# Performance work log

Hardware: AMD Instinct MI355X
Metric: run time of the kernel (lower is better)

## Reference

```python
import jax, jax.numpy as jnp
import numpy as np

N_NODES = 100000
N_EDGES = 1600000
NODE_DIM = 128
EDGE_DIM = 48
GLOBAL_DIM = 64
N_GRAPHS = 64
HIDDEN = 256


def setup_inputs() -> dict:
    key = jax.random.key(0)
    ks = jax.random.split(key, 9)
    nodes = jax.random.normal(ks[0], (N_NODES, NODE_DIM), dtype=jnp.float32)
    edges = jax.random.normal(ks[1], (N_EDGES, EDGE_DIM), dtype=jnp.float32)
    edge_index = jax.random.randint(ks[2], (2, N_EDGES), 0, N_NODES, dtype=jnp.int64)
    batch = jnp.sort(jax.random.randint(ks[3], (N_NODES,), 0, N_GRAPHS, dtype=jnp.int64))
    graph_globals = jax.random.normal(ks[4], (N_GRAPHS, GLOBAL_DIM), dtype=jnp.float32)
    in_dim = NODE_DIM + EDGE_DIM + GLOBAL_DIM
    s1 = 1.0 / np.sqrt(in_dim)
    s2 = 1.0 / np.sqrt(HIDDEN)
    W1 = jax.random.uniform(ks[5], (in_dim, HIDDEN), minval=-s1, maxval=s1, dtype=jnp.float32)
    b1 = jax.random.uniform(ks[6], (HIDDEN,), minval=-s1, maxval=s1, dtype=jnp.float32)
    W2 = jax.random.uniform(ks[7], (HIDDEN, NODE_DIM), minval=-s2, maxval=s2, dtype=jnp.float32)
    b2 = jax.random.uniform(ks[8], (NODE_DIM,), minval=-s2, maxval=s2, dtype=jnp.float32)
    return {"nodes": nodes, "edges": edges, "edge_index": edge_index, "batch": batch,
            "graph_globals": graph_globals, "W1": W1, "b1": b1, "W2": W2, "b2": b2}


def reference(nodes, edges, edge_index, batch, graph_globals, W1, b1, W2, b2):
    recv = edge_index[1]
    # scatter-add edge messages to receiving nodes: [N, edge_dim]
    agg = jax.ops.segment_sum(edges, recv, num_segments=N_NODES)
    # gather per-graph globals to nodes: [N, global_dim]
    u = graph_globals[batch]
    x = jnp.concatenate([nodes, agg, u], axis=1)  # [N, node+edge+global]
    h = jax.nn.relu(x @ W1 + b1)
    return h @ W2 + b2  # new node features [N, node_dim]
```

## Files before the change

kernel.cpp:

```cpp
#include <hip/hip_runtime.h>
#include <hip/hip_bf16.h>
#include <stdint.h>

#define N_NODES   100000
#define N_EDGES   1600000
#define NODE_DIM  128
#define EDGE_DIM  48
#define GLOBAL_DIM 64
#define HIDDEN    256
#define KDIM      256
#define OUT_DIM   128

#define N_PAD     100352
#define SCAN_BLKS 98

#define W1P_OFF   0
#define W1P_BYTES (KDIM * HIDDEN * 2)
#define W2P_OFF   (W1P_OFF + W1P_BYTES)
#define W2P_BYTES (HIDDEN * OUT_DIM * 2)
#define CNT_OFF   (W2P_OFF + W2P_BYTES)
#define CNT_BYTES (N_PAD * 4)
#define OFF_OFF   (CNT_OFF + CNT_BYTES)
#define BSUM_OFF  (OFF_OFF + CNT_BYTES)
#define BSUM_BYTES 512
#define BEX_OFF   (BSUM_OFF + BSUM_BYTES)
#define RANK_OFF  (BEX_OFF + BSUM_BYTES)
#define RANK_BYTES (N_EDGES * 4)
#define EIDS_OFF  (RANK_OFF + RANK_BYTES)

typedef short  short4_t  __attribute__((ext_vector_type(4)));
typedef short  short8_t  __attribute__((ext_vector_type(8)));
typedef float  floatx4   __attribute__((ext_vector_type(4)));

__device__ __forceinline__ short f2bf(float f) {
    union { float f; uint32_t u; } x; x.f = f;
    uint32_t r = (x.u + 0x7FFFu + ((x.u >> 16) & 1u)) >> 16;
    return (short)r;
}

__global__ void pack_w1(const float* __restrict__ W1, short* __restrict__ dst) {
    int tid = blockIdx.x * 256 + threadIdx.x;
    int k = tid >> 8, n = tid & 255;
    float v = (k < 240) ? W1[k * 256 + n] : 0.0f;
    int kg = k >> 5, kr = k & 31, quad = kr >> 3, j = kr & 7;
    int nt = n >> 4, nl = n & 15, lane = (quad << 4) | nl;
    dst[(((kg * 16 + nt) * 64) + lane) * 8 + j] = f2bf(v);
}

__global__ void pack_w2(const float* __restrict__ W2, short* __restrict__ dst) {
    int tid = blockIdx.x * 256 + threadIdx.x;
    int k = tid >> 7, n = tid & 127;
    float v = W2[k * 128 + n];
    int kg = k >> 5, kr = k & 31, quad = kr >> 3, j = kr & 7;
    int nt = n >> 4, nl = n & 15, lane = (quad << 4) | nl;
    dst[(((kg * 8 + nt) * 64) + lane) * 8 + j] = f2bf(v);
}

__global__ void count_kernel(const int4* __restrict__ recv4, int* __restrict__ cnt,
                             int4* __restrict__ rank4) {
    int tid = blockIdx.x * 256 + threadIdx.x;
    if (tid >= N_EDGES / 4) return;
    int4 r = recv4[tid];
    int4 k;
    k.x = atomicAdd(&cnt[r.x], 1);
    k.y = atomicAdd(&cnt[r.y], 1);
    k.z = atomicAdd(&cnt[r.z], 1);
    k.w = atomicAdd(&cnt[r.w], 1);
    rank4[tid] = k;
}

__global__ void scan_bsum(const int4* __restrict__ cnt4, int* __restrict__ bsum) {
    int4 v = cnt4[blockIdx.x * 256 + threadIdx.x];
    int s = v.x + v.y + v.z + v.w;
    #pragma unroll
    for (int d = 32; d; d >>= 1) s += __shfl_down(s, d);
    __shared__ int ws[4];
    if ((threadIdx.x & 63) == 0) ws[threadIdx.x >> 6] = s;
    __syncthreads();
    if (threadIdx.x == 0) bsum[blockIdx.x] = ws[0] + ws[1] + ws[2] + ws[3];
}

__global__ void scan_top(const int* __restrict__ bsum, int* __restrict__ bex) {
    __shared__ int tmp[128];
    int t = threadIdx.x;
    int v = (t < SCAN_BLKS) ? bsum[t] : 0;
    tmp[t] = v;
    __syncthreads();
    #pragma unroll
    for (int d = 1; d < 128; d <<= 1) {
        int add = (t >= d) ? tmp[t - d] : 0;
        __syncthreads();
        tmp[t] += add;
        __syncthreads();
    }
    if (t < SCAN_BLKS) bex[t] = tmp[t] - v;
}

__global__ void scan_write(const int4* __restrict__ cnt4, const int* __restrict__ bex,
                           int4* __restrict__ off4) {
    int t = threadIdx.x, b = blockIdx.x;
    int4 v = cnt4[b * 256 + t];
    int tsum = v.x + v.y + v.z + v.w;
    int lane = t & 63, w = t >> 6;
    int x = tsum;
    #pragma unroll
    for (int d = 1; d < 64; d <<= 1) {
        int y = __shfl_up(x, d);
        if (lane >= d) x += y;
    }
    __shared__ int wsum[4];
    if (lane == 63) wsum[w] = x;
    __syncthreads();
    int wb = 0;
    if (w > 0) wb += wsum[0];
    if (w > 1) wb += wsum[1];
    if (w > 2) wb += wsum[2];
    int base = bex[b] + wb + (x - tsum);
    int4 o;
    o.x = base;
    o.y = base + v.x;
    o.z = base + v.x + v.y;
    o.w = base + v.x + v.y + v.z;
    off4[b * 256 + t] = o;
}

__global__ void fill_kernel(const int4* __restrict__ recv4, const int4* __restrict__ rank4,
                            const int* __restrict__ off, int* __restrict__ eids) {
    int tid = blockIdx.x * 256 + threadIdx.x;
    if (tid >= N_EDGES / 4) return;
    int4 r = recv4[tid];
    int4 k = rank4[tid];
    int e = tid * 4;
    eids[off[r.x] + k.x] = e + 0;
    eids[off[r.y] + k.y] = e + 1;
    eids[off[r.z] + k.z] = e + 2;
    eids[off[r.w] + k.w] = e + 3;
}

#define LDS_W 264
__global__ __launch_bounds__(256, 2)
void mlp_kernel(const float* __restrict__ nodes,
                const int* __restrict__ eids,
                const int* __restrict__ off,
                const float4* __restrict__ edges4,
                const int* __restrict__ batch,
                const float* __restrict__ gg,
                const short8_t* __restrict__ w1p,
                const short8_t* __restrict__ w2p,
                const float* __restrict__ b1,
                const float* __restrict__ b2,
                float* __restrict__ out) {
    __shared__ short xt[64 * LDS_W];

    const int t = threadIdx.x;
    const int m0 = blockIdx.x * 64;
    const int w    = t >> 6;
    const int lane = t & 63;

    {
        int sub = lane / 12;
        int c4g = lane - sub * 12;
        bool gact = lane < 48;
        #pragma unroll
        for (int qi = 0; qi < 4; ++qi) {
            int r = w * 16 + qi * 4 + sub;
            int node = m0 + r;
            int o = 0, c = 0;
            if (gact && node < N_NODES) {
                o = off[node];
                c = off[node + 1] - o;
            }
            int cmax = c;
            #pragma unroll
            for (int d = 1; d < 64; d <<= 1) cmax = max(cmax, __shfl_xor(cmax, d));
            float4 acc = make_float4(0.f, 0.f, 0.f, 0.f);
            int i = 0;
            for (; i + 2 <= cmax; i += 2) {
                float4 v0 = make_float4(0.f, 0.f, 0.f, 0.f);
                float4 v1 = make_float4(0.f, 0.f, 0.f, 0.f);
                if (i < c) {
                    int e0 = eids[o + i];
                    v0 = edges4[(size_t)e0 * 12 + c4g];
                }
                if (i + 1 < c) {
                    int e1 = eids[o + i + 1];
                    v1 = edges4[(size_t)e1 * 12 + c4g];
                }
                acc.x += v0.x + v1.x; acc.y += v0.y + v1.y;
                acc.z += v0.z + v1.z; acc.w += v0.w + v1.w;
            }
            if (i < cmax && i < c) {
                int e0 = eids[o + i];
                float4 v0 = edges4[(size_t)e0 * 12 + c4g];
                acc.x += v0.x; acc.y += v0.y; acc.z += v0.z; acc.w += v0.w;
            }
            if (gact) {
                short4_t s;
                s.x = f2bf(acc.x); s.y = f2bf(acc.y);
                s.z = f2bf(acc.z); s.w = f2bf(acc.w);
                *(short4_t*)(&xt[r * LDS_W + (32 + c4g) * 4]) = s;
            }
        }
    }

    const float4* nodes4 = (const float4*)nodes;
    const float4* gg4    = (const float4*)gg;

    #pragma unroll
    for (int i = 0; i < 8; ++i) {
        int f = t + 256 * i;
        int r = f >> 5, c4 = f & 31;
        int node = m0 + r;
        float4 v = make_float4(0.f, 0.f, 0.f, 0.f);
        if (node < N_NODES) v = nodes4[node * 32 + c4];
        short4_t s; s.x = f2bf(v.x); s.y = f2bf(v.y); s.z = f2bf(v.z); s.w = f2bf(v.w);
        *(short4_t*)(&xt[r * LDS_W + c4 * 4]) = s;
    }
    #pragma unroll
    for (int i = 0; i < 4; ++i) {
        int f = t + 256 * i;
        int r = f >> 4, c4 = f & 15;
        int node = m0 + r;
        float4 v = make_float4(0.f, 0.f, 0.f, 0.f);
        if (node < N_NODES) { int g = batch[node]; v = gg4[g * 16 + c4]; }
        short4_t s; s.x = f2bf(v.x); s.y = f2bf(v.y); s.z = f2bf(v.z); s.w = f2bf(v.w);
        *(short4_t*)(&xt[r * LDS_W + (44 + c4) * 4]) = s;
    }
    {
        int r = t >> 2, c4 = t & 3;
        short4_t s; s.x = 0; s.y = 0; s.z = 0; s.w = 0;
        *(short4_t*)(&xt[r * LDS_W + (60 + c4) * 4]) = s;
    }
    __syncthreads();

    const int q  = lane >> 4;
    const int ln = lane & 15;

    floatx4 acc[4][4];
    #pragma unroll
    for (int a = 0; a < 4; ++a)
        #pragma unroll
        for (int b = 0; b < 4; ++b) acc[a][b] = 0.0f;

    #pragma unroll
    for (int kg = 0; kg < 8; ++kg) {
        short8_t A[4], B[4];
        #pragma unroll
        for (int mt = 0; mt < 4; ++mt)
            A[mt] = *(const short8_t*)(&xt[(mt * 16 + ln) * LDS_W + kg * 32 + q * 8]);
        #pragma unroll
        for (int ntl = 0; ntl < 4; ++ntl) {
            int nt = w * 4 + ntl;
            B[ntl] = (const short8_t&)w1p[(kg * 16 + nt) * 64 + lane];
        }
        #pragma unroll
        for (int mt = 0; mt < 4; ++mt)
            #pragma unroll
            for (int ntl = 0; ntl < 4; ++ntl)
                acc[mt][ntl] = __builtin_amdgcn_mfma_f32_16x16x32_bf16(
                    A[mt], B[ntl], acc[mt][ntl], 0, 0, 0);
    }

    float b1v[4];
    #pragma unroll
    for (int ntl = 0; ntl < 4; ++ntl) b1v[ntl] = b1[w * 64 + ntl * 16 + ln];

    __syncthreads();

    #pragma unroll
    for (int mt = 0; mt < 4; ++mt)
        #pragma unroll
        for (int ntl = 0; ntl < 4; ++ntl)
            #pragma unroll
            for (int r = 0; r < 4; ++r) {
                float v = acc[mt][ntl][r] + b1v[ntl];
                v = fmaxf(v, 0.0f);
                xt[(mt * 16 + q * 4 + r) * LDS_W + w * 64 + ntl * 16 + ln] = f2bf(v);
            }
    __syncthreads();

    floatx4 acc2[4][2];
    #pragma unroll
    for (int a = 0; a < 4; ++a)
        #pragma unroll
        for (int b = 0; b < 2; ++b) acc2[a][b] = 0.0f;

    #pragma unroll
    for (int kg = 0; kg < 8; ++kg) {
        short8_t A[4], B[2];
        #pragma unroll
        for (int mt = 0; mt < 4; ++mt)
            A[mt] = *(const short8_t*)(&xt[(mt * 16 + ln) * LDS_W + kg * 32 + q * 8]);
        #pragma unroll
        for (int ntl = 0; ntl < 2; ++ntl) {
            int nt = w * 2 + ntl;
            B[ntl] = (const short8_t&)w2p[(kg * 8 + nt) * 64 + lane];
        }
        #pragma unroll
        for (int mt = 0; mt < 4; ++mt)
            #pragma unroll
            for (int ntl = 0; ntl < 2; ++ntl)
                acc2[mt][ntl] = __builtin_amdgcn_mfma_f32_16x16x32_bf16(
                    A[mt], B[ntl], acc2[mt][ntl], 0, 0, 0);
    }

    float b2v[2];
    #pragma unroll
    for (int ntl = 0; ntl < 2; ++ntl) b2v[ntl] = b2[w * 32 + ntl * 16 + ln];

    #pragma unroll
    for (int mt = 0; mt < 4; ++mt)
        #pragma unroll
        for (int ntl = 0; ntl < 2; ++ntl)
            #pragma unroll
            for (int r = 0; r < 4; ++r) {
                int node = m0 + mt * 16 + q * 4 + r;
                if (node < N_NODES)
                    out[node * 128 + w * 32 + ntl * 16 + ln] = acc2[mt][ntl][r] + b2v[ntl];
            }
}

extern "C" void kernel_launch(void* const* d_in, const int* in_sizes, int n_in,
                              void* d_out, int out_size, void* d_ws, size_t ws_size,
                              hipStream_t stream) {
    const float* nodes = (const float*)d_in[0];
    const float* edges = (const float*)d_in[1];
    const int* edge_index = (const int*)d_in[2];
    const int* batch = (const int*)d_in[3];
    const float* gg = (const float*)d_in[4];
    const float* W1 = (const float*)d_in[5];
    const float* b1 = (const float*)d_in[6];
    const float* W2 = (const float*)d_in[7];
    const float* b2 = (const float*)d_in[8];
    float* out = (float*)d_out;

    char* ws = (char*)d_ws;
    short* w1p  = (short*)(ws + W1P_OFF);
    short* w2p  = (short*)(ws + W2P_OFF);
    int*   cnt  = (int*)  (ws + CNT_OFF);
    int*   off  = (int*)  (ws + OFF_OFF);
    int*   bsum = (int*)  (ws + BSUM_OFF);
    int*   bex  = (int*)  (ws + BEX_OFF);
    int*   rank = (int*)  (ws + RANK_OFF);
    int*   eids = (int*)  (ws + EIDS_OFF);
    const int* recv = edge_index + N_EDGES;

    hipMemsetAsync(cnt, 0, CNT_BYTES, stream);
    pack_w1<<<256, 256, 0, stream>>>(W1, w1p);
    pack_w2<<<128, 256, 0, stream>>>(W2, w2p);
    count_kernel<<<(N_EDGES / 4 + 255) / 256, 256, 0, stream>>>(
        (const int4*)recv, cnt, (int4*)rank);
    scan_bsum<<<SCAN_BLKS, 256, 0, stream>>>((const int4*)cnt, bsum);
    scan_top<<<1, 128, 0, stream>>>(bsum, bex);
    scan_write<<<SCAN_BLKS, 256, 0, stream>>>((const int4*)cnt, bex, (int4*)off);
    fill_kernel<<<(N_EDGES / 4 + 255) / 256, 256, 0, stream>>>(
        (const int4*)recv, (const int4*)rank, off, eids);
    mlp_kernel<<<(N_NODES + 63) / 64, 256, 0, stream>>>(
        nodes, eids, off, (const float4*)edges, batch, gg,
        (const short8_t*)w1p, (const short8_t*)w2p, b1, b2, out);
}
```

Before: 741.8 us.

## Fuse prep kernels, drop rank buffer via atomic fill, unroll gather, raise occupancy

Merges the W1/W2 packing and the count memset into one prep kernel, which removes two launches and a memset. The count kernel no longer stores per-edge ranks. The fill kernel instead takes slots by atomically incrementing a copy of the offsets, which saves a 6.4 MB write and read but makes the order of edges within each node nondeterministic. The edge gather loop now issues four loads per iteration instead of two, and launch bounds are raised to 4 blocks per CU, which may force register spilling in the MLP.

```diff
diff --git a/kernel.cpp b/kernel.cpp
--- a/kernel.cpp
+++ b/kernel.cpp
@@ -21,12 +21,11 @@
 #define CNT_OFF   (W2P_OFF + W2P_BYTES)
 #define CNT_BYTES (N_PAD * 4)
 #define OFF_OFF   (CNT_OFF + CNT_BYTES)
-#define BSUM_OFF  (OFF_OFF + CNT_BYTES)
+#define OFF2_OFF  (OFF_OFF + CNT_BYTES)
+#define BSUM_OFF  (OFF2_OFF + CNT_BYTES)
 #define BSUM_BYTES 512
 #define BEX_OFF   (BSUM_OFF + BSUM_BYTES)
-#define RANK_OFF  (BEX_OFF + BSUM_BYTES)
-#define RANK_BYTES (N_EDGES * 4)
-#define EIDS_OFF  (RANK_OFF + RANK_BYTES)
+#define EIDS_OFF  (BEX_OFF + BSUM_BYTES)
 
 typedef short  short4_t  __attribute__((ext_vector_type(4)));
 typedef short  short8_t  __attribute__((ext_vector_type(8)));
@@ -38,35 +37,39 @@
     return (short)r;
 }
 
-__global__ void pack_w1(const float* __restrict__ W1, short* __restrict__ dst) {
-    int tid = blockIdx.x * 256 + threadIdx.x;
-    int k = tid >> 8, n = tid & 255;
-    float v = (k < 240) ? W1[k * 256 + n] : 0.0f;
-    int kg = k >> 5, kr = k & 31, quad = kr >> 3, j = kr & 7;
-    int nt = n >> 4, nl = n & 15, lane = (quad << 4) | nl;
-    dst[(((kg * 16 + nt) * 64) + lane) * 8 + j] = f2bf(v);
-}
-
-__global__ void pack_w2(const float* __restrict__ W2, short* __restrict__ dst) {
-    int tid = blockIdx.x * 256 + threadIdx.x;
-    int k = tid >> 7, n = tid & 127;
-    float v = W2[k * 128 + n];
-    int kg = k >> 5, kr = k & 31, quad = kr >> 3, j = kr & 7;
-    int nt = n >> 4, nl = n & 15, lane = (quad << 4) | nl;
-    dst[(((kg * 8 + nt) * 64) + lane) * 8 + j] = f2bf(v);
-}
-
-__global__ void count_kernel(const int4* __restrict__ recv4, int* __restrict__ cnt,
-                             int4* __restrict__ rank4) {
+__global__ void prep_kernel(const float* __restrict__ W1, short* __restrict__ w1p,
+                            const float* __restrict__ W2, short* __restrict__ w2p,
+                            int4* __restrict__ cnt4) {
+    int b = blockIdx.x;
+    if (b < 256) {
+        int tid = b * 256 + threadIdx.x;
+        int k = tid >> 8, n = tid & 255;
+        float v = (k < 240) ? W1[k * 256 + n] : 0.0f;
+        int kg = k >> 5, kr = k & 31, quad = kr >> 3, j = kr & 7;
+        int nt = n >> 4, nl = n & 15, lane = (quad << 4) | nl;
+        w1p[(((kg * 16 + nt) * 64) + lane) * 8 + j] = f2bf(v);
+    } else if (b < 384) {
+        int tid = (b - 256) * 256 + threadIdx.x;
+        int k = tid >> 7, n = tid & 127;
+        float v = W2[k * 128 + n];
+        int kg = k >> 5, kr = k & 31, quad = kr >> 3, j = kr & 7;
+        int nt = n >> 4, nl = n & 15, lane = (quad << 4) | nl;
+        w2p[(((kg * 8 + nt) * 64) + lane) * 8 + j] = f2bf(v);
+    } else {
+        int i = (b - 384) * 256 + threadIdx.x;
+        int4 z; z.x = 0; z.y = 0; z.z = 0; z.w = 0;
+        cnt4[i] = z;
+    }
+}
+
+__global__ void count_kernel(const int4* __restrict__ recv4, int* __restrict__ cnt) {
     int tid = blockIdx.x * 256 + threadIdx.x;
     if (tid >= N_EDGES / 4) return;
     int4 r = recv4[tid];
-    int4 k;
-    k.x = atomicAdd(&cnt[r.x], 1);
-    k.y = atomicAdd(&cnt[r.y], 1);
-    k.z = atomicAdd(&cnt[r.z], 1);
-    k.w = atomicAdd(&cnt[r.w], 1);
-    rank4[tid] = k;
+    atomicAdd(&cnt[r.x], 1);
+    atomicAdd(&cnt[r.y], 1);
+    atomicAdd(&cnt[r.z], 1);
+    atomicAdd(&cnt[r.w], 1);
 }
 
 __global__ void scan_bsum(const int4* __restrict__ cnt4, int* __restrict__ bsum) {
@@ -97,7 +100,7 @@
 }
 
 __global__ void scan_write(const int4* __restrict__ cnt4, const int* __restrict__ bex,
-                           int4* __restrict__ off4) {
+                           int4* __restrict__ off4, int4* __restrict__ off2_4) {
     int t = threadIdx.x, b = blockIdx.x;
     int4 v = cnt4[b * 256 + t];
     int tsum = v.x + v.y + v.z + v.w;
@@ -122,23 +125,23 @@
     o.z = base + v.x + v.y;
     o.w = base + v.x + v.y + v.z;
     off4[b * 256 + t] = o;
-}
-
-__global__ void fill_kernel(const int4* __restrict__ recv4, const int4* __restrict__ rank4,
-                            const int* __restrict__ off, int* __restrict__ eids) {
+    off2_4[b * 256 + t] = o;
+}
+
+__global__ void fill_kernel(const int4* __restrict__ recv4, int* __restrict__ off2,
+                            int* __restrict__ eids) {
     int tid = blockIdx.x * 256 + threadIdx.x;
     if (tid >= N_EDGES / 4) return;
     int4 r = recv4[tid];
-    int4 k = rank4[tid];
     int e = tid * 4;
-    eids[off[r.x] + k.x] = e + 0;
-    eids[off[r.y] + k.y] = e + 1;
-    eids[off[r.z] + k.z] = e + 2;
-    eids[off[r.w] + k.w] = e + 3;
+    eids[atomicAdd(&off2[r.x], 1)] = e + 0;
+    eids[atomicAdd(&off2[r.y], 1)] = e + 1;
+    eids[atomicAdd(&off2[r.z], 1)] = e + 2;
+    eids[atomicAdd(&off2[r.w], 1)] = e + 3;
 }
 
 #define LDS_W 264
-__global__ __launch_bounds__(256, 2)
+__global__ __launch_bounds__(256, 4)
 void mlp_kernel(const float* __restrict__ nodes,
                 const int* __restrict__ eids,
                 const int* __restrict__ off,
@@ -174,25 +177,20 @@
             #pragma unroll
             for (int d = 1; d < 64; d <<= 1) cmax = max(cmax, __shfl_xor(cmax, d));
             float4 acc = make_float4(0.f, 0.f, 0.f, 0.f);
-            int i = 0;
-            for (; i + 2 <= cmax; i += 2) {
-                float4 v0 = make_float4(0.f, 0.f, 0.f, 0.f);
-                float4 v1 = make_float4(0.f, 0.f, 0.f, 0.f);
-                if (i < c) {
-                    int e0 = eids[o + i];
-                    v0 = edges4[(size_t)e0 * 12 + c4g];
-                }
-                if (i + 1 < c) {
-                    int e1 = eids[o + i + 1];
-                    v1 = edges4[(size_t)e1 * 12 + c4g];
-                }
-                acc.x += v0.x + v1.x; acc.y += v0.y + v1.y;
-                acc.z += v0.z + v1.z; acc.w += v0.w + v1.w;
-            }
-            if (i < cmax && i < c) {
-                int e0 = eids[o + i];
-                float4 v0 = edges4[(size_t)e0 * 12 + c4g];
-                acc.x += v0.x; acc.y += v0.y; acc.z += v0.z; acc.w += v0.w;
+            const float4 z4 = make_float4(0.f, 0.f, 0.f, 0.f);
+            for (int i = 0; i < cmax; i += 4) {
+                int e0 = (i + 0 < c) ? eids[o + i + 0] : -1;
+                int e1 = (i + 1 < c) ? eids[o + i + 1] : -1;
+                int e2 = (i + 2 < c) ? eids[o + i + 2] : -1;
+                int e3 = (i + 3 < c) ? eids[o + i + 3] : -1;
+                float4 v0 = (e0 >= 0) ? edges4[(size_t)e0 * 12 + c4g] : z4;
+                float4 v1 = (e1 >= 0) ? edges4[(size_t)e1 * 12 + c4g] : z4;
+                float4 v2 = (e2 >= 0) ? edges4[(size_t)e2 * 12 + c4g] : z4;
+                float4 v3 = (e3 >= 0) ? edges4[(size_t)e3 * 12 + c4g] : z4;
+                acc.x += (v0.x + v1.x) + (v2.x + v3.x);
+                acc.y += (v0.y + v1.y) + (v2.y + v3.y);
+                acc.z += (v0.z + v1.z) + (v2.z + v3.z);
+                acc.w += (v0.w + v1.w) + (v2.w + v3.w);
             }
             if (gact) {
                 short4_t s;
@@ -339,22 +337,21 @@
     short* w2p  = (short*)(ws + W2P_OFF);
     int*   cnt  = (int*)  (ws + CNT_OFF);
     int*   off  = (int*)  (ws + OFF_OFF);
+    int*   off2 = (int*)  (ws + OFF2_OFF);
     int*   bsum = (int*)  (ws + BSUM_OFF);
     int*   bex  = (int*)  (ws + BEX_OFF);
-    int*   rank = (int*)  (ws + RANK_OFF);
     int*   eids = (int*)  (ws + EIDS_OFF);
     const int* recv = edge_index + N_EDGES;
 
-    hipMemsetAsync(cnt, 0, CNT_BYTES, stream);
-    pack_w1<<<256, 256, 0, stream>>>(W1, w1p);
-    pack_w2<<<128, 256, 0, stream>>>(W2, w2p);
+    prep_kernel<<<482, 256, 0, stream>>>(W1, w1p, W2, w2p, (int4*)cnt);
     count_kernel<<<(N_EDGES / 4 + 255) / 256, 256, 0, stream>>>(
-        (const int4*)recv, cnt, (int4*)rank);
+        (const int4*)recv, cnt);
     scan_bsum<<<SCAN_BLKS, 256, 0, stream>>>((const int4*)cnt, bsum);
     scan_top<<<1, 128, 0, stream>>>(bsum, bex);
-    scan_write<<<SCAN_BLKS, 256, 0, stream>>>((const int4*)cnt, bex, (int4*)off);
+    scan_write<<<SCAN_BLKS, 256, 0, stream>>>((const int4*)cnt, bex,
+                                              (int4*)off, (int4*)off2);
     fill_kernel<<<(N_EDGES / 4 + 255) / 256, 256, 0, stream>>>(
-        (const int4*)recv, (const int4*)rank, off, eids);
+        (const int4*)recv, off2, eids);
     mlp_kernel<<<(N_NODES + 63) / 64, 256, 0, stream>>>(
         nodes, eids, off, (const float4*)edges, batch, gg,
         (const short8_t*)w1p, (const short8_t*)w2p, b1, b2, out);
```

Measured after the change: 732.4 us. No clear change (-1.3%).
